# Kernel optimization log

Hardware: AMD Instinct MI355X
Metric: run time of the kernel (lower is better)

## Reference

```python
import jax, jax.numpy as jnp
import numpy as np

B, S, D, H = 4, 1024, 1024, 16
DH = D // H  # 64, per-head dim; FFN hidden = 2048
DFF = 2048

def setup_inputs() -> dict:
    key = jax.random.key(0)
    ks = jax.random.split(key, 6)
    x = jax.random.normal(ks[0], (B, S, D), dtype=jnp.float32)
    # Per-head q/k/v projection weights, stacked over heads: [H, D, DH].
    # Equivalent math to n_heads separate SelfAttentionLayer(d_head) calls + concat.
    sc_in = 1.0 / np.sqrt(D)
    Wq = jax.random.normal(ks[1], (H, D, DH), dtype=jnp.float32) * sc_in
    Wk = jax.random.normal(ks[2], (H, D, DH), dtype=jnp.float32) * sc_in
    Wv = jax.random.normal(ks[3], (H, D, DH), dtype=jnp.float32) * sc_in
    W1 = jax.random.normal(ks[4], (D, DFF), dtype=jnp.float32) * sc_in
    b1 = jnp.zeros((DFF,), dtype=jnp.float32)
    W2 = jax.random.normal(ks[5], (DFF, D), dtype=jnp.float32) * (1.0 / np.sqrt(DFF))
    b2 = jnp.zeros((D,), dtype=jnp.float32)
    return {"x": x, "Wq": Wq, "Wk": Wk, "Wv": Wv,
            "W1": W1, "b1": b1, "W2": W2, "b2": b2}

def reference(x, Wq, Wk, Wv, W1, b1, W2, b2):
    # Batched multi-head self-attention (math-equivalent to the per-head loop + concat).
    q = jnp.einsum('bsd,hde->bhse', x, Wq)          # [B,H,S,DH]
    k = jnp.einsum('bsd,hde->bhse', x, Wk)
    v = jnp.einsum('bsd,hde->bhse', x, Wv)
    scale = 1.0 / jnp.sqrt(jnp.asarray(q.shape[-1], q.dtype))
    scores = jnp.einsum('bhqe,bhke->bhqk', q, k) * scale  # [B,H,S,S]
    attn = jax.nn.softmax(scores, axis=-1)
    o = jnp.einsum('bhqk,bhke->bhqe', attn, v)      # [B,H,S,DH]
    h1 = o.transpose(0, 2, 1, 3).reshape(x.shape[0], x.shape[1], -1)  # concat heads -> [B,S,D]
    # FCLayer(2048, d): Dense(2048, relu) -> Dense(d)
    y = jax.nn.relu(h1 @ W1 + b1) @ W2 + b2
    return y
```

## Files before the change

### kernel.cpp

```cpp
#include <hip/hip_runtime.h>
#include <hip/hip_bf16.h>


typedef unsigned short u16;
typedef __attribute__((ext_vector_type(8))) short bfrag8;
typedef __attribute__((ext_vector_type(4))) float f32x4;
typedef __attribute__((ext_vector_type(16))) float f32x16;
typedef __attribute__((ext_vector_type(4))) int ix4;

constexpr int Bb = 4, Ss = 1024, Dd = 1024, Hh = 16, DFF = 2048;
constexpr float QSCALE = 0.18033688011112042f;

__device__ __forceinline__ u16 f2bf(float f) {
  unsigned u = __float_as_uint(f);
  return (u16)((u + 0x7fffu + ((u >> 16) & 1u)) >> 16);
}

__device__ __forceinline__ void gload16(const void* g, void* l) {
  __builtin_amdgcn_global_load_lds(
      (const __attribute__((address_space(1))) unsigned int*)g,
      (__attribute__((address_space(3))) unsigned int*)l, 16, 0, 0);
}

__device__ __forceinline__ int xcd_swz() {
  const int id = blockIdx.y * gridDim.x + blockIdx.x;
  const int cpx = (gridDim.x * gridDim.y) >> 3;
  return (id & 7) * cpx + (id >> 3);
}

__global__ __launch_bounds__(256) void cvt_bf16(const float* __restrict__ in,
                                                u16* __restrict__ out, int n4) {
  int i = blockIdx.x * 256 + threadIdx.x;
  if (i >= n4) return;
  float4 v = ((const float4*)in)[i];
  ushort4 o = make_ushort4(f2bf(v.x), f2bf(v.y), f2bf(v.z), f2bf(v.w));
  *(ushort4*)(out + (size_t)i * 4) = o;
}

__device__ __forceinline__ void transpose64(const float* __restrict__ in,
                                            u16* __restrict__ out,
                                            int R, int C, int r0, int c0) {
  __shared__ float tile[64][65];
  const int t = threadIdx.x, cl = t & 63, rq = t >> 6;
#pragma unroll
  for (int i = 0; i < 16; ++i) {
    int rl = rq * 16 + i;
    tile[rl][cl] = in[(size_t)(r0 + rl) * C + c0 + cl];
  }
  __syncthreads();
#pragma unroll
  for (int i = 0; i < 16; ++i) {
    int oc = rq * 16 + i;
    out[(size_t)(c0 + oc) * R + r0 + cl] = f2bf(tile[cl][oc]);
  }
}

__global__ __launch_bounds__(256) void transpose_cvt(const float* __restrict__ in,
                                                     u16* __restrict__ out,
                                                     int R, int C) {
  transpose64(in, out, R, C, blockIdx.x * 64, blockIdx.y * 64);
}

__global__ __launch_bounds__(256) void qkv_transpose_cvt(
    const float* __restrict__ Wq, const float* __restrict__ Wk,
    const float* __restrict__ Wv, u16* __restrict__ out) {
  const int z = blockIdx.y;
  const int which = z >> 4, h = z & 15;
  const float* in = (which == 0 ? Wq : which == 1 ? Wk : Wv) + (size_t)h * 1024 * 64;
  u16* o = out + (size_t)z * 64 * 1024;
  transpose64(in, o, 1024, 64, blockIdx.x * 64, 0);
}

__global__ __launch_bounds__(256) void vt_transpose(const u16* __restrict__ in,
                                                    u16* __restrict__ out) {
  __shared__ float tile[64][65];
  const int hb = blockIdx.y, s0 = blockIdx.x * 64;
  const int t = threadIdx.x, cl = t & 63, rq = t >> 6;
#pragma unroll
  for (int i = 0; i < 16; ++i) {
    const int rl = rq * 16 + i;
    tile[rl][cl] = __uint_as_float(
        (unsigned)in[((size_t)hb * 1024 + s0 + rl) * 64 + cl] << 16);
  }
  __syncthreads();
#pragma unroll
  for (int i = 0; i < 16; ++i) {
    const int oc = rq * 16 + i;
    out[((size_t)hb * 64 + oc) * 1024 + s0 + cl] =
        (u16)(__float_as_uint(tile[cl][oc]) >> 16);
  }
}

template <int EPI>
__global__ __launch_bounds__(256) void mfma_gemm(
    const u16* __restrict__ A, const u16* __restrict__ Bt,
    const float* __restrict__ bias, void* __restrict__ Cout, int N, int K) {
  __shared__ alignas(16) u16 Asm[128 * 32];
  __shared__ alignas(16) u16 Bsm[128 * 32];
  const int tid = threadIdx.x;
  const int wid = tid >> 6, lane = tid & 63;
  const int nid = xcd_swz();
  const int m0 = (nid / gridDim.x) * 128, n0 = (nid % gridDim.x) * 128;
  const int wr = wid >> 1, wc = wid & 1;
  const int fr = lane & 15, krow = lane >> 4;

  const int srow = tid >> 2;
  const int sk = (tid & 3) * 8;
  const u16* ga0 = A + (size_t)(m0 + srow) * K + sk;
  const u16* ga1 = A + (size_t)(m0 + srow + 64) * K + sk;
  const u16* gb0 = Bt + (size_t)(n0 + srow) * K + sk;
  const u16* gb1 = Bt + (size_t)(n0 + srow + 64) * K + sk;
  char* lA0 = (char*)Asm + tid * 16;
  char* lA1 = lA0 + 4096;
  char* lB0 = (char*)Bsm + tid * 16;
  char* lB1 = lB0 + 4096;

  f32x4 acc[4][4];
#pragma unroll
  for (int i = 0; i < 4; ++i)
#pragma unroll
    for (int j = 0; j < 4; ++j) acc[i][j] = (f32x4){0.f, 0.f, 0.f, 0.f};

  const char* pa = (const char*)Asm + (wr * 64 + fr) * 64 + krow * 16;
  const char* pb = (const char*)Bsm + (wc * 64 + fr) * 64 + krow * 16;

  for (int kt = 0; kt < K / 32; ++kt) {
    __syncthreads();
    gload16(ga0 + kt * 32, lA0);
    gload16(ga1 + kt * 32, lA1);
    gload16(gb0 + kt * 32, lB0);
    gload16(gb1 + kt * 32, lB1);
    __syncthreads();

    bfrag8 af[4], bfv[4];
#pragma unroll
    for (int i = 0; i < 4; ++i) af[i] = *(const bfrag8*)(pa + i * 1024);
#pragma unroll
    for (int j = 0; j < 4; ++j) bfv[j] = *(const bfrag8*)(pb + j * 1024);
#pragma unroll
    for (int i = 0; i < 4; ++i)
#pragma unroll
      for (int j = 0; j < 4; ++j)
        acc[i][j] = __builtin_amdgcn_mfma_f32_16x16x32_bf16(af[i], bfv[j], acc[i][j], 0, 0, 0);
  }

  const int orow = (lane >> 4) * 4;
  const int ocol = lane & 15;
#pragma unroll
  for (int i = 0; i < 4; ++i) {
#pragma unroll
    for (int j = 0; j < 4; ++j) {
      const int gn = n0 + wc * 64 + j * 16 + ocol;
      const int gm0 = m0 + wr * 64 + i * 16 + orow;
      if (EPI == 0) {
        const int which = gn >> 10, hh = (gn >> 6) & 15, e = gn & 63;
        const int bb = gm0 >> 10, s0 = gm0 & 1023;
        const int hb = hh * 4 + bb;
        u16* oq = (u16*)Cout + (size_t)which * 4194304 +
                  ((size_t)hb * 1024 + s0) * 64 + e;
        const float sc = (which == 0) ? QSCALE : 1.f;
#pragma unroll
        for (int r = 0; r < 4; ++r) oq[r * 64] = f2bf(acc[i][j][r] * sc);
      } else if (EPI == 1) {
#pragma unroll
        for (int r = 0; r < 4; ++r) {
          float v = fmaxf(acc[i][j][r] + bias[gn], 0.f);
          ((u16*)Cout)[(size_t)(gm0 + r) * N + gn] = f2bf(v);
        }
      } else {
#pragma unroll
        for (int r = 0; r < 4; ++r)
          ((float*)Cout)[(size_t)(gm0 + r) * N + gn] = acc[i][j][r] + bias[gn];
      }
    }
  }
}

__global__ __launch_bounds__(256) void mfma_gemm_n64(
    const u16* __restrict__ A, const u16* __restrict__ Bt,
    const float* __restrict__ bias, float* __restrict__ Cout, int N, int K) {
  __shared__ alignas(16) u16 Asm[128 * 32];
  __shared__ alignas(16) u16 Bsm[64 * 32];
  const int tid = threadIdx.x;
  const int wid = tid >> 6, lane = tid & 63;
  const int nid = xcd_swz();
  const int m0 = (nid / gridDim.x) * 128, n0 = (nid % gridDim.x) * 64;
  const int fr = lane & 15, krow = lane >> 4;

  const int srow = tid >> 2;
  const int sk = (tid & 3) * 8;
  const u16* ga0 = A + (size_t)(m0 + srow) * K + sk;
  const u16* ga1 = A + (size_t)(m0 + srow + 64) * K + sk;
  const u16* gb0 = Bt + (size_t)(n0 + srow) * K + sk;
  char* lA0 = (char*)Asm + tid * 16;
  char* lA1 = lA0 + 4096;
  char* lB0 = (char*)Bsm + tid * 16;

  f32x4 acc[2][4];
#pragma unroll
  for (int i = 0; i < 2; ++i)
#pragma unroll
    for (int j = 0; j < 4; ++j) acc[i][j] = (f32x4){0.f, 0.f, 0.f, 0.f};

  const char* pa = (const char*)Asm + (wid * 32 + fr) * 64 + krow * 16;
  const char* pb = (const char*)Bsm + fr * 64 + krow * 16;

  for (int kt = 0; kt < K / 32; ++kt) {
    __syncthreads();
    gload16(ga0 + kt * 32, lA0);
    gload16(ga1 + kt * 32, lA1);
    gload16(gb0 + kt * 32, lB0);
    __syncthreads();

    bfrag8 af[2], bfv[4];
#pragma unroll
    for (int i = 0; i < 2; ++i) af[i] = *(const bfrag8*)(pa + i * 1024);
#pragma unroll
    for (int j = 0; j < 4; ++j) bfv[j] = *(const bfrag8*)(pb + j * 1024);
#pragma unroll
    for (int i = 0; i < 2; ++i)
#pragma unroll
      for (int j = 0; j < 4; ++j)
        acc[i][j] = __builtin_amdgcn_mfma_f32_16x16x32_bf16(af[i], bfv[j], acc[i][j], 0, 0, 0);
  }

  const int orow = (lane >> 4) * 4;
  const int ocol = lane & 15;
#pragma unroll
  for (int i = 0; i < 2; ++i)
#pragma unroll
    for (int j = 0; j < 4; ++j) {
      const int gn = n0 + j * 16 + ocol;
      const int gm0 = m0 + wid * 32 + i * 16 + orow;
#pragma unroll
      for (int r = 0; r < 4; ++r)
        Cout[(size_t)(gm0 + r) * N + gn] = acc[i][j][r] + bias[gn];
    }
}

__global__ __launch_bounds__(256, 2) void attn_mfma32(
    const u16* __restrict__ qb, const u16* __restrict__ kb,
    const u16* __restrict__ vtb, u16* __restrict__ h1) {
  const int wid = threadIdx.x >> 6, lane = threadIdx.x & 63;
  const int nid = xcd_swz();
  const int qx = nid & 7, hb = nid >> 3;
  const int h = hb >> 2, b = hb & 3;
  const int q0 = qx * 128 + wid * 32;
  const int ql = lane & 31, hi = lane >> 5;

  const u16* Qp = qb + ((size_t)hb * 1024 + q0 + ql) * 64 + hi * 8;
  const u16* Kp = kb + (size_t)hb * 65536 + (size_t)ql * 64 + hi * 8;
  const u16* Vp = vtb + (size_t)hb * 65536 + (size_t)ql * 1024 + hi * 8;

  bfrag8 qf[4];
#pragma unroll
  for (int st = 0; st < 4; ++st) qf[st] = *(const bfrag8*)(Qp + st * 16);

  f32x16 po0, po1;
#pragma unroll
  for (int i = 0; i < 16; ++i) { po0[i] = 0.f; po1[i] = 0.f; }
  float mrun = -1e30f, lrun = 0.f;

  bfrag8 kA[8], kB[8], vv[8];

#define LOADK(dst, kt)                                                         \
  {                                                                            \
    _Pragma("unroll") for (int st = 0; st < 4; ++st) {                         \
      dst[st]     = *(const bfrag8*)(Kp + (size_t)(kt) * 4096 + st * 16);      \
      dst[4 + st] = *(const bfrag8*)(Kp + (size_t)(kt) * 4096 + 2048 + st * 16); \
    }                                                                          \
  }
#define LOADV(dst, kt)                                                         \
  {                                                                            \
    _Pragma("unroll") for (int st = 0; st < 4; ++st) {                         \
      dst[st]     = *(const bfrag8*)(Vp + (kt) * 64 + st * 16);                \
      dst[4 + st] = *(const bfrag8*)(Vp + 32768 + (kt) * 64 + st * 16);        \
    }                                                                          \
  }

#define PACK4(dst, p, base)                                                    \
  {                                                                            \
    int a0, a1, b0, b1;                                                        \
    asm("v_cvt_pk_bf16_f32 %0, %1, %2" : "=v"(a0)                              \
        : "v"(p[base + 0]), "v"(p[base + 1]));                                 \
    asm("v_cvt_pk_bf16_f32 %0, %1, %2" : "=v"(a1)                              \
        : "v"(p[base + 2]), "v"(p[base + 3]));                                 \
    asm("v_cvt_pk_bf16_f32 %0, %1, %2" : "=v"(b0)                              \
        : "v"(p[base + 4]), "v"(p[base + 5]));                                 \
    asm("v_cvt_pk_bf16_f32 %0, %1, %2" : "=v"(b1)                              \
        : "v"(p[base + 6]), "v"(p[base + 7]));                                 \
    asm("v_permlane32_swap_b32 %0, %1" : "+v"(a0), "+v"(b0));                  \
    asm("v_permlane32_swap_b32 %0, %1" : "+v"(a1), "+v"(b1));                  \
    ix4 t = (ix4){a0, a1, b0, b1};                                             \
    dst = __builtin_bit_cast(bfrag8, t);                                       \
  }

#define STEP(kf)                                                               \
  {                                                                            \
    f32x16 pa0, pa1;                                                           \
    _Pragma("unroll") for (int i = 0; i < 16; ++i) { pa0[i] = 0.f; pa1[i] = 0.f; } \
    __builtin_amdgcn_s_setprio(1);                                             \
    _Pragma("unroll") for (int st = 0; st < 4; ++st) {                         \
      pa0 = __builtin_amdgcn_mfma_f32_32x32x16_bf16(kf[st], qf[st], pa0, 0, 0, 0); \
      pa1 = __builtin_amdgcn_mfma_f32_32x32x16_bf16(kf[4 + st], qf[st], pa1, 0, 0, 0); \
    }                                                                          \
    __builtin_amdgcn_s_setprio(0);                                             \
    float t4[8];                                                               \
    _Pragma("unroll") for (int g = 0; g < 4; ++g) {                            \
      t4[g] = fmaxf(fmaxf(pa0[4 * g], pa0[4 * g + 1]),                         \
                    fmaxf(pa0[4 * g + 2], pa0[4 * g + 3]));                    \
      t4[4 + g] = fmaxf(fmaxf(pa1[4 * g], pa1[4 * g + 1]),                     \
                        fmaxf(pa1[4 * g + 2], pa1[4 * g + 3]));                \
    }                                                                          \
    float cm = fmaxf(fmaxf(fmaxf(t4[0], t4[1]), fmaxf(t4[2], t4[3])),          \
                     fmaxf(fmaxf(t4[4], t4[5]), fmaxf(t4[6], t4[7])));         \
    cm = fmaxf(cm, __shfl_xor(cm, 32));                                        \
    if (__any(cm > mrun + 8.f)) {    \
      const float mnew = fmaxf(mrun, cm);                                      \
      const float scl = exp2f(mrun - mnew);                                    \
      mrun = mnew;                                                             \
      lrun *= scl;                                                             \
      po0 *= scl;                                                              \
      po1 *= scl;                                                              \
    }                                                                          \
    _Pragma("unroll") for (int i = 0; i < 16; ++i) {                           \
      pa0[i] = exp2f(pa0[i] - mrun);                                           \
      pa1[i] = exp2f(pa1[i] - mrun);                                           \
    }                                                                          \
    float s4[8];                                                               \
    _Pragma("unroll") for (int g = 0; g < 4; ++g) {                            \
      s4[g] = (pa0[4 * g] + pa0[4 * g + 1]) + (pa0[4 * g + 2] + pa0[4 * g + 3]); \
      s4[4 + g] = (pa1[4 * g] + pa1[4 * g + 1]) + (pa1[4 * g + 2] + pa1[4 * g + 3]); \
    }                                                                          \
    float psum = ((s4[0] + s4[1]) + (s4[2] + s4[3])) +                         \
                 ((s4[4] + s4[5]) + (s4[6] + s4[7]));                          \
    psum += __shfl_xor(psum, 32);                                              \
    lrun += psum;                                                              \
    bfrag8 pf00, pf01, pf10, pf11;                                             \
    PACK4(pf00, pa0, 0);                                                       \
    PACK4(pf01, pa0, 8);                                                       \
    PACK4(pf10, pa1, 0);                                                       \
    PACK4(pf11, pa1, 8);                                                       \
    __builtin_amdgcn_s_setprio(1);                                             \
    po0 = __builtin_amdgcn_mfma_f32_32x32x16_bf16(vv[0], pf00, po0, 0, 0, 0);  \
    po0 = __builtin_amdgcn_mfma_f32_32x32x16_bf16(vv[1], pf01, po0, 0, 0, 0);  \
    po0 = __builtin_amdgcn_mfma_f32_32x32x16_bf16(vv[2], pf10, po0, 0, 0, 0);  \
    po0 = __builtin_amdgcn_mfma_f32_32x32x16_bf16(vv[3], pf11, po0, 0, 0, 0);  \
    po1 = __builtin_amdgcn_mfma_f32_32x32x16_bf16(vv[4], pf00, po1, 0, 0, 0);  \
    po1 = __builtin_amdgcn_mfma_f32_32x32x16_bf16(vv[5], pf01, po1, 0, 0, 0);  \
    po1 = __builtin_amdgcn_mfma_f32_32x32x16_bf16(vv[6], pf10, po1, 0, 0, 0);  \
    po1 = __builtin_amdgcn_mfma_f32_32x32x16_bf16(vv[7], pf11, po1, 0, 0, 0);  \
    __builtin_amdgcn_s_setprio(0);                                             \
  }

  LOADK(kA, 0);
  for (int kt = 0; kt < 16; kt += 2) {
    LOADV(vv, kt);
    LOADK(kB, kt + 1);
    STEP(kA);
    LOADV(vv, kt + 1);
    if (kt + 2 < 16) LOADK(kA, kt + 2);
    STEP(kB);
  }
#undef LOADK
#undef LOADV
#undef PACK4
#undef STEP

  const float inv = 1.f / lrun;
  u16* orow = h1 + ((size_t)(b * 1024 + q0 + ql)) * 1024 + h * 64 + hi * 4;
#pragma unroll
  for (int r4 = 0; r4 < 4; ++r4) {
    ushort4 o0 = make_ushort4(
        f2bf(po0[r4 * 4 + 0] * inv), f2bf(po0[r4 * 4 + 1] * inv),
        f2bf(po0[r4 * 4 + 2] * inv), f2bf(po0[r4 * 4 + 3] * inv));
    *(ushort4*)(orow + r4 * 8) = o0;
    ushort4 o1 = make_ushort4(
        f2bf(po1[r4 * 4 + 0] * inv), f2bf(po1[r4 * 4 + 1] * inv),
        f2bf(po1[r4 * 4 + 2] * inv), f2bf(po1[r4 * 4 + 3] * inv));
    *(ushort4*)(orow + 32 + r4 * 8) = o1;
  }
}

extern "C" void kernel_launch(void* const* d_in, const int* in_sizes, int n_in,
                              void* d_out, int out_size, void* d_ws, size_t ws_size,
                              hipStream_t stream) {
  const float* x  = (const float*)d_in[0];
  const float* Wq = (const float*)d_in[1];
  const float* Wk = (const float*)d_in[2];
  const float* Wv = (const float*)d_in[3];
  const float* W1 = (const float*)d_in[4];
  const float* b1 = (const float*)d_in[5];
  const float* W2 = (const float*)d_in[6];
  const float* b2 = (const float*)d_in[7];

  const size_t MB = 1u << 20;
  char* w = (char*)d_ws;
  u16* qkvb  = (u16*)w;
  u16* vtb   = (u16*)(w + 24 * MB);
  u16* Xb    = (u16*)(w + 32 * MB);
  u16* Wqkvt = (u16*)(w + 40 * MB);
  u16* W1t   = (u16*)(w + 46 * MB);
  u16* W2t   = (u16*)(w + 50 * MB);
  u16* h1b   = (u16*)(w + 54 * MB);
  u16* ffb   = (u16*)(w + 62 * MB);

  cvt_bf16<<<4096, 256, 0, stream>>>(x, Xb, 1048576);
  qkv_transpose_cvt<<<dim3(16, 48), 256, 0, stream>>>(Wq, Wk, Wv, Wqkvt);
  transpose_cvt<<<dim3(16, 32), 256, 0, stream>>>(W1, W1t, 1024, 2048);
  transpose_cvt<<<dim3(32, 16), 256, 0, stream>>>(W2, W2t, 2048, 1024);

  mfma_gemm<0><<<dim3(24, 32), 256, 0, stream>>>(Xb, Wqkvt, nullptr, qkvb, 3072, 1024);
  vt_transpose<<<dim3(16, 64), 256, 0, stream>>>(qkvb + 8388608, vtb);
  attn_mfma32<<<dim3(8, 64), 256, 0, stream>>>(qkvb, qkvb + 4194304, vtb, h1b);
  mfma_gemm<1><<<dim3(16, 32), 256, 0, stream>>>(h1b, W1t, b1, ffb, 2048, 1024);
  mfma_gemm_n64<<<dim3(16, 32), 256, 0, stream>>>(ffb, W2t, b2, (float*)d_out, 1024, 2048);
}
```

Baseline: 269.8 us.

## Double-buffer GEMM LDS tiles and split attention KV into two partitions

Both MFMA GEMM kernels get double-buffered LDS tiles, so the next K-tile's global-to-LDS loads are issued before the current tile is computed, with one barrier per tile. The attention kernel is split along the key dimension into two halves (flash-decoding style). This doubles the grid to 1024 blocks and raises the occupancy hint to 4, and each half writes an unnormalized partial output plus (max, sum) stats. A new combine kernel merges the two partials into h1. In exchange it adds an extra launch and partial-output traffic, plus bf16 rounding of the unnormalized partials.

```diff
diff --git a/kernel.cpp b/kernel.cpp
--- a/kernel.cpp
+++ b/kernel.cpp
@@ -14,6 +14,10 @@
 __device__ __forceinline__ u16 f2bf(float f) {
   unsigned u = __float_as_uint(f);
   return (u16)((u + 0x7fffu + ((u >> 16) & 1u)) >> 16);
+}
+
+__device__ __forceinline__ float bf2f(u16 u) {
+  return __uint_as_float((unsigned)u << 16);
 }
 
 __device__ __forceinline__ void gload16(const void* g, void* l) {
@@ -79,8 +83,7 @@
 #pragma unroll
   for (int i = 0; i < 16; ++i) {
     const int rl = rq * 16 + i;
-    tile[rl][cl] = __uint_as_float(
-        (unsigned)in[((size_t)hb * 1024 + s0 + rl) * 64 + cl] << 16);
+    tile[rl][cl] = bf2f(in[((size_t)hb * 1024 + s0 + rl) * 64 + cl]);
   }
   __syncthreads();
 #pragma unroll
@@ -95,8 +98,8 @@
 __global__ __launch_bounds__(256) void mfma_gemm(
     const u16* __restrict__ A, const u16* __restrict__ Bt,
     const float* __restrict__ bias, void* __restrict__ Cout, int N, int K) {
-  __shared__ alignas(16) u16 Asm[128 * 32];
-  __shared__ alignas(16) u16 Bsm[128 * 32];
+  __shared__ alignas(16) u16 Asm[2][128 * 32];
+  __shared__ alignas(16) u16 Bsm[2][128 * 32];
   const int tid = threadIdx.x;
   const int wid = tid >> 6, lane = tid & 63;
   const int nid = xcd_swz();
@@ -110,10 +113,6 @@
   const u16* ga1 = A + (size_t)(m0 + srow + 64) * K + sk;
   const u16* gb0 = Bt + (size_t)(n0 + srow) * K + sk;
   const u16* gb1 = Bt + (size_t)(n0 + srow + 64) * K + sk;
-  char* lA0 = (char*)Asm + tid * 16;
-  char* lA1 = lA0 + 4096;
-  char* lB0 = (char*)Bsm + tid * 16;
-  char* lB1 = lB0 + 4096;
 
   f32x4 acc[4][4];
 #pragma unroll
@@ -121,28 +120,43 @@
 #pragma unroll
     for (int j = 0; j < 4; ++j) acc[i][j] = (f32x4){0.f, 0.f, 0.f, 0.f};
 
-  const char* pa = (const char*)Asm + (wr * 64 + fr) * 64 + krow * 16;
-  const char* pb = (const char*)Bsm + (wc * 64 + fr) * 64 + krow * 16;
-
-  for (int kt = 0; kt < K / 32; ++kt) {
+#define STAGE(buf, kt)                                                         \
+  {                                                                            \
+    char* dA = (char*)Asm[buf] + tid * 16;                                     \
+    char* dB = (char*)Bsm[buf] + tid * 16;                                     \
+    gload16(ga0 + (kt) * 32, dA);                                              \
+    gload16(ga1 + (kt) * 32, dA + 4096);                                       \
+    gload16(gb0 + (kt) * 32, dB);                                              \
+    gload16(gb1 + (kt) * 32, dB + 4096);                                       \
+  }
+#define COMPUTE(buf)                                                           \
+  {                                                                            \
+    const char* pa = (const char*)Asm[buf] + (wr * 64 + fr) * 64 + krow * 16;  \
+    const char* pb = (const char*)Bsm[buf] + (wc * 64 + fr) * 64 + krow * 16;  \
+    bfrag8 af[4], bfv[4];                                                      \
+    _Pragma("unroll") for (int i = 0; i < 4; ++i)                              \
+        af[i] = *(const bfrag8*)(pa + i * 1024);                               \
+    _Pragma("unroll") for (int j = 0; j < 4; ++j)                              \
+        bfv[j] = *(const bfrag8*)(pb + j * 1024);                              \
+    _Pragma("unroll") for (int i = 0; i < 4; ++i)                              \
+        _Pragma("unroll") for (int j = 0; j < 4; ++j)                          \
+            acc[i][j] = __builtin_amdgcn_mfma_f32_16x16x32_bf16(               \
+                af[i], bfv[j], acc[i][j], 0, 0, 0);                            \
+  }
+
+  const int NT = K / 32;
+  STAGE(0, 0);
+  __syncthreads();
+  for (int kt = 0; kt < NT; kt += 2) {
+    if (kt + 1 < NT) STAGE(1, kt + 1);
+    COMPUTE(0);
     __syncthreads();
-    gload16(ga0 + kt * 32, lA0);
-    gload16(ga1 + kt * 32, lA1);
-    gload16(gb0 + kt * 32, lB0);
-    gload16(gb1 + kt * 32, lB1);
+    if (kt + 2 < NT) STAGE(0, kt + 2);
+    COMPUTE(1);
     __syncthreads();
-
-    bfrag8 af[4], bfv[4];
-#pragma unroll
-    for (int i = 0; i < 4; ++i) af[i] = *(const bfrag8*)(pa + i * 1024);
-#pragma unroll
-    for (int j = 0; j < 4; ++j) bfv[j] = *(const bfrag8*)(pb + j * 1024);
-#pragma unroll
-    for (int i = 0; i < 4; ++i)
-#pragma unroll
-      for (int j = 0; j < 4; ++j)
-        acc[i][j] = __builtin_amdgcn_mfma_f32_16x16x32_bf16(af[i], bfv[j], acc[i][j], 0, 0, 0);
-  }
+  }
+#undef STAGE
+#undef COMPUTE
 
   const int orow = (lane >> 4) * 4;
   const int ocol = lane & 15;
@@ -179,8 +193,8 @@
 __global__ __launch_bounds__(256) void mfma_gemm_n64(
     const u16* __restrict__ A, const u16* __restrict__ Bt,
     const float* __restrict__ bias, float* __restrict__ Cout, int N, int K) {
-  __shared__ alignas(16) u16 Asm[128 * 32];
-  __shared__ alignas(16) u16 Bsm[64 * 32];
+  __shared__ alignas(16) u16 Asm[2][128 * 32];
+  __shared__ alignas(16) u16 Bsm[2][64 * 32];
   const int tid = threadIdx.x;
   const int wid = tid >> 6, lane = tid & 63;
   const int nid = xcd_swz();
@@ -192,9 +206,6 @@
   const u16* ga0 = A + (size_t)(m0 + srow) * K + sk;
   const u16* ga1 = A + (size_t)(m0 + srow + 64) * K + sk;
   const u16* gb0 = Bt + (size_t)(n0 + srow) * K + sk;
-  char* lA0 = (char*)Asm + tid * 16;
-  char* lA1 = lA0 + 4096;
-  char* lB0 = (char*)Bsm + tid * 16;
 
   f32x4 acc[2][4];
 #pragma unroll
@@ -202,27 +213,42 @@
 #pragma unroll
     for (int j = 0; j < 4; ++j) acc[i][j] = (f32x4){0.f, 0.f, 0.f, 0.f};
 
-  const char* pa = (const char*)Asm + (wid * 32 + fr) * 64 + krow * 16;
-  const char* pb = (const char*)Bsm + fr * 64 + krow * 16;
-
-  for (int kt = 0; kt < K / 32; ++kt) {
+#define STAGE(buf, kt)                                                         \
+  {                                                                            \
+    char* dA = (char*)Asm[buf] + tid * 16;                                     \
+    char* dB = (char*)Bsm[buf] + tid * 16;                                     \
+    gload16(ga0 + (kt) * 32, dA);                                              \
+    gload16(ga1 + (kt) * 32, dA + 4096);                                       \
+    gload16(gb0 + (kt) * 32, dB);                                              \
+  }
+#define COMPUTE(buf)                                                           \
+  {                                                                            \
+    const char* pa = (const char*)Asm[buf] + (wid * 32 + fr) * 64 + krow * 16; \
+    const char* pb = (const char*)Bsm[buf] + fr * 64 + krow * 16;              \
+    bfrag8 af[2], bfv[4];                                                      \
+    _Pragma("unroll") for (int i = 0; i < 2; ++i)                              \
+        af[i] = *(const bfrag8*)(pa + i * 1024);                               \
+    _Pragma("unroll") for (int j = 0; j < 4; ++j)                              \
+        bfv[j] = *(const bfrag8*)(pb + j * 1024);                              \
+    _Pragma("unroll") for (int i = 0; i < 2; ++i)                              \
+        _Pragma("unroll") for (int j = 0; j < 4; ++j)                          \
+            acc[i][j] = __builtin_amdgcn_mfma_f32_16x16x32_bf16(               \
+                af[i], bfv[j], acc[i][j], 0, 0, 0);                            \
+  }
+
+  const int NT = K / 32;
+  STAGE(0, 0);
+  __syncthreads();
+  for (int kt = 0; kt < NT; kt += 2) {
+    if (kt + 1 < NT) STAGE(1, kt + 1);
+    COMPUTE(0);
     __syncthreads();
-    gload16(ga0 + kt * 32, lA0);
-    gload16(ga1 + kt * 32, lA1);
-    gload16(gb0 + kt * 32, lB0);
+    if (kt + 2 < NT) STAGE(0, kt + 2);
+    COMPUTE(1);
     __syncthreads();
-
-    bfrag8 af[2], bfv[4];
-#pragma unroll
-    for (int i = 0; i < 2; ++i) af[i] = *(const bfrag8*)(pa + i * 1024);
-#pragma unroll
-    for (int j = 0; j < 4; ++j) bfv[j] = *(const bfrag8*)(pb + j * 1024);
-#pragma unroll
-    for (int i = 0; i < 2; ++i)
-#pragma unroll
-      for (int j = 0; j < 4; ++j)
-        acc[i][j] = __builtin_amdgcn_mfma_f32_16x16x32_bf16(af[i], bfv[j], acc[i][j], 0, 0, 0);
-  }
+  }
+#undef STAGE
+#undef COMPUTE
 
   const int orow = (lane >> 4) * 4;
   const int ocol = lane & 15;
@@ -238,19 +264,22 @@
     }
 }
 
-__global__ __launch_bounds__(256, 2) void attn_mfma32(
+__global__ __launch_bounds__(256, 4) void attn_mfma32(
     const u16* __restrict__ qb, const u16* __restrict__ kb,
-    const u16* __restrict__ vtb, u16* __restrict__ h1) {
+    const u16* __restrict__ vtb, u16* __restrict__ pO,
+    float2* __restrict__ ml) {
   const int wid = threadIdx.x >> 6, lane = threadIdx.x & 63;
   const int nid = xcd_swz();
-  const int qx = nid & 7, hb = nid >> 3;
-  const int h = hb >> 2, b = hb & 3;
+  const int qx = nid & 7;
+  const int split = (nid >> 3) & 1;
+  const int hb = nid >> 4;
+  const int h = hb >> 2, b = hb & 3;  (void)h; (void)b;
   const int q0 = qx * 128 + wid * 32;
   const int ql = lane & 31, hi = lane >> 5;
 
   const u16* Qp = qb + ((size_t)hb * 1024 + q0 + ql) * 64 + hi * 8;
-  const u16* Kp = kb + (size_t)hb * 65536 + (size_t)ql * 64 + hi * 8;
-  const u16* Vp = vtb + (size_t)hb * 65536 + (size_t)ql * 1024 + hi * 8;
+  const u16* Kp = kb + (size_t)hb * 65536 + (size_t)(split * 512 + ql) * 64 + hi * 8;
+  const u16* Vp = vtb + (size_t)hb * 65536 + (size_t)ql * 1024 + split * 512 + hi * 8;
 
   bfrag8 qf[4];
 #pragma unroll
@@ -354,12 +383,12 @@
   }
 
   LOADK(kA, 0);
-  for (int kt = 0; kt < 16; kt += 2) {
+  for (int kt = 0; kt < 8; kt += 2) {
     LOADV(vv, kt);
     LOADK(kB, kt + 1);
     STEP(kA);
     LOADV(vv, kt + 1);
-    if (kt + 2 < 16) LOADK(kA, kt + 2);
+    if (kt + 2 < 8) LOADK(kA, kt + 2);
     STEP(kB);
   }
 #undef LOADK
@@ -367,19 +396,46 @@
 #undef PACK4
 #undef STEP
 
-  const float inv = 1.f / lrun;
-  u16* orow = h1 + ((size_t)(b * 1024 + q0 + ql)) * 1024 + h * 64 + hi * 4;
+  const size_t prow = ((size_t)split * 64 + hb) * 1024 + q0 + ql;
+  u16* orow = pO + prow * 64 + hi * 4;
 #pragma unroll
   for (int r4 = 0; r4 < 4; ++r4) {
-    ushort4 o0 = make_ushort4(
-        f2bf(po0[r4 * 4 + 0] * inv), f2bf(po0[r4 * 4 + 1] * inv),
-        f2bf(po0[r4 * 4 + 2] * inv), f2bf(po0[r4 * 4 + 3] * inv));
+    ushort4 o0 = make_ushort4(f2bf(po0[r4 * 4 + 0]), f2bf(po0[r4 * 4 + 1]),
+                              f2bf(po0[r4 * 4 + 2]), f2bf(po0[r4 * 4 + 3]));
     *(ushort4*)(orow + r4 * 8) = o0;
-    ushort4 o1 = make_ushort4(
-        f2bf(po1[r4 * 4 + 0] * inv), f2bf(po1[r4 * 4 + 1] * inv),
-        f2bf(po1[r4 * 4 + 2] * inv), f2bf(po1[r4 * 4 + 3] * inv));
+    ushort4 o1 = make_ushort4(f2bf(po1[r4 * 4 + 0]), f2bf(po1[r4 * 4 + 1]),
+                              f2bf(po1[r4 * 4 + 2]), f2bf(po1[r4 * 4 + 3]));
     *(ushort4*)(orow + 32 + r4 * 8) = o1;
   }
+  if (hi == 0) ml[prow] = make_float2(mrun, lrun);
+}
+
+__global__ __launch_bounds__(256) void attn_combine(
+    const u16* __restrict__ pO, const float2* __restrict__ ml,
+    u16* __restrict__ h1) {
+  const int gid = blockIdx.x * 256 + threadIdx.x;
+  const int row = gid >> 3;
+  const int e0 = (gid & 7) * 8;
+  const int hb = row >> 10, q = row & 1023;
+  const int h = hb >> 2, b = hb & 3;
+  const float2 a = ml[row];
+  const float2 c = ml[65536 + row];
+  const float m = fmaxf(a.x, c.x);
+  const float w0 = exp2f(a.x - m), w1 = exp2f(c.x - m);
+  const float inv = 1.f / (a.y * w0 + c.y * w1);
+  const float f0 = w0 * inv, f1 = w1 * inv;
+  const ushort4* p0 = (const ushort4*)(pO + (size_t)row * 64 + e0);
+  const ushort4* p1 = (const ushort4*)(pO + (size_t)(65536 + row) * 64 + e0);
+  ushort4 x0 = p0[0], x1 = p0[1], y0 = p1[0], y1 = p1[1];
+  u16* op = h1 + ((size_t)(b * 1024 + q)) * 1024 + h * 64 + e0;
+  ushort4 o0 = make_ushort4(
+      f2bf(bf2f(x0.x) * f0 + bf2f(y0.x) * f1), f2bf(bf2f(x0.y) * f0 + bf2f(y0.y) * f1),
+      f2bf(bf2f(x0.z) * f0 + bf2f(y0.z) * f1), f2bf(bf2f(x0.w) * f0 + bf2f(y0.w) * f1));
+  ushort4 o1 = make_ushort4(
+      f2bf(bf2f(x1.x) * f0 + bf2f(y1.x) * f1), f2bf(bf2f(x1.y) * f0 + bf2f(y1.y) * f1),
+      f2bf(bf2f(x1.z) * f0 + bf2f(y1.z) * f1), f2bf(bf2f(x1.w) * f0 + bf2f(y1.w) * f1));
+  *(ushort4*)op = o0;
+  *(ushort4*)(op + 4) = o1;
 }
 
 extern "C" void kernel_launch(void* const* d_in, const int* in_sizes, int n_in,
@@ -404,6 +460,8 @@
   u16* W2t   = (u16*)(w + 50 * MB);
   u16* h1b   = (u16*)(w + 54 * MB);
   u16* ffb   = (u16*)(w + 62 * MB);
+  u16* pOb   = (u16*)(w + 78 * MB);
+  float2* mlb = (float2*)(w + 94 * MB);
 
   cvt_bf16<<<4096, 256, 0, stream>>>(x, Xb, 1048576);
   qkv_transpose_cvt<<<dim3(16, 48), 256, 0, stream>>>(Wq, Wk, Wv, Wqkvt);
@@ -412,7 +470,8 @@
 
   mfma_gemm<0><<<dim3(24, 32), 256, 0, stream>>>(Xb, Wqkvt, nullptr, qkvb, 3072, 1024);
   vt_transpose<<<dim3(16, 64), 256, 0, stream>>>(qkvb + 8388608, vtb);
-  attn_mfma32<<<dim3(8, 64), 256, 0, stream>>>(qkvb, qkvb + 4194304, vtb, h1b);
+  attn_mfma32<<<dim3(16, 64), 256, 0, stream>>>(qkvb, qkvb + 4194304, vtb, pOb, mlb);
+  attn_combine<<<2048, 256, 0, stream>>>(pOb, mlb, h1b);
   mfma_gemm<1><<<dim3(16, 32), 256, 0, stream>>>(h1b, W1t, b1, ffb, 2048, 1024);
   mfma_gemm_n64<<<dim3(16, 32), 256, 0, stream>>>(ffb, W2t, b2, (float*)d_out, 1024, 2048);
 }
```

Result: slower. 336.7 us (+24.8%).
